# Kernel optimization log

Measured on AMD Instinct MI355X. Metric: run time of the kernel, lower is better.

Reference implementation:

```python
import jax, jax.numpy as jnp
import numpy as np

N = 50000          # total nodes
G = 16             # graphs in batch
NPG = N // G       # nodes per graph (3125)
E_RAND = 600000    # random intra-graph edges
EPG = E_RAND // G  # edges per graph
IN, HID, OUT = 128, 256, 256
LN_EPS = 1e-5


def setup_inputs() -> dict:
    key = jax.random.key(0)
    ks = jax.random.split(key, 20)
    features = jax.random.normal(ks[0], (N, IN), jnp.float32)
    # random edges constrained inside each graph block, then self loops (add_self_loop)
    off = (jnp.arange(E_RAND, dtype=jnp.int32) // EPG) * NPG
    src = jax.random.randint(ks[1], (E_RAND,), 0, NPG, dtype=jnp.int32) + off
    dst = jax.random.randint(ks[2], (E_RAND,), 0, NPG, dtype=jnp.int32) + off
    self_ids = jnp.arange(N, dtype=jnp.int32)
    edge_src = jnp.concatenate([src, self_ids])
    edge_dst = jnp.concatenate([dst, self_ids])
    graph_ids = (jnp.arange(N, dtype=jnp.int32) // NPG)

    def lin(k, i, o):
        return jax.random.normal(k, (i, o), jnp.float32) * 0.02

    dims = [(IN, HID), (HID, HID), (HID, OUT)]
    inp = {
        "features": features,
        "edge_src": edge_src,
        "edge_dst": edge_dst,
        "graph_ids": graph_ids,
    }
    for l, (di, do) in enumerate(dims):
        inp[f"Wself{l}"] = lin(ks[3 + 4 * l], di, do)
        inp[f"Wneigh{l}"] = lin(ks[4 + 4 * l], di, do)
        inp[f"b{l}"] = jnp.zeros((do,), jnp.float32)
        inp[f"g{l}"] = jnp.ones((do,), jnp.float32)
        inp[f"be{l}"] = jnp.zeros((do,), jnp.float32)
    return inp


def _layer_norm(x, g, b):
    m = jnp.mean(x, axis=-1, keepdims=True)
    v = jnp.mean((x - m) ** 2, axis=-1, keepdims=True)
    return (x - m) * jax.lax.rsqrt(v + LN_EPS) * g + b


def reference(features, edge_src, edge_dst, graph_ids,
              Wself0, Wneigh0, b0, g0, be0,
              Wself1, Wneigh1, b1, g1, be1,
              Wself2, Wneigh2, b2, g2, be2):
    n = features.shape[0]
    # in-degree (self loops guarantee >= 1)
    deg = jax.ops.segment_sum(jnp.ones_like(edge_dst, dtype=features.dtype), edge_dst, num_segments=n)
    deg_inv = (1.0 / deg)[:, None]

    def sage(h, Ws, Wn, b, g, be):
        # mean-aggregate neighbor (src) features at dst: gather + segment_sum
        agg = jax.ops.segment_sum(h[edge_src], edge_dst, num_segments=n) * deg_inv
        out = h @ Ws + agg @ Wn + b          # SAGEConv(mean): fc_self + fc_neigh
        return jax.nn.elu(_layer_norm(out, g, be))

    h = sage(features, Wself0, Wneigh0, b0, g0, be0)
    h = sage(h, Wself1, Wneigh1, b1, g1, be1)
    h = sage(h, Wself2, Wneigh2, b2, g2, be2)

    # per-graph mean readout (torch.mean over each graph's nodes)
    cnt = jax.ops.segment_sum(jnp.ones((n,), h.dtype), graph_ids, num_segments=G)
    hg = jax.ops.segment_sum(h, graph_ids, num_segments=G) / cnt[:, None]
    return h, hg
```

## Files before the change

### kernel.cpp

```cpp
#include <hip/hip_runtime.h>
#include <hip/hip_bf16.h>

constexpr int DOUT = 256;

typedef __bf16 bf16x8 __attribute__((ext_vector_type(8)));
typedef float f32x4 __attribute__((ext_vector_type(4)));

__device__ inline float bf2f(ushort u) {
  return __uint_as_float((unsigned)u << 16);
}
__device__ inline ushort f2bf(float f) {
  unsigned b = __float_as_uint(f);
  return (ushort)((b + 0x7FFF + ((b >> 16) & 1)) >> 16);
}
__device__ inline float bflo(int v) {
  return __uint_as_float((unsigned)v << 16);
}
__device__ inline float bfhi(int v) {
  return __uint_as_float((unsigned)v & 0xffff0000u);
}
__device__ inline int packbf(float a, float b) {
  return (int)((unsigned)f2bf(a) | ((unsigned)f2bf(b) << 16));
}

__device__ inline int xcd_swizzle(int bid, int nwg) {
  int q = nwg >> 3, r = nwg & 7;
  int xcd = bid & 7, idx = bid >> 3;
  return (xcd < r ? xcd * (q + 1) : r * (q + 1) + (xcd - r) * q) + idx;
}

__global__ __launch_bounds__(256) void k_cnt(const int* __restrict__ edst,
                                             int* __restrict__ deg, int E, int Eb,
                                             const int* __restrict__ gid,
                                             int* __restrict__ gcnt, int n, int G) {
  __shared__ int h[16];
  int b = blockIdx.x;
  if (b < Eb) {
    int t = b * 256 + threadIdx.x;
    if (t < E) atomicAdd(&deg[edst[t]], 1);
  } else {
    b -= Eb;
    int t = threadIdx.x;
    if (t < G) h[t] = 0;
    __syncthreads();
    int i = b * 256 + t;
    if (i < n) atomicAdd(&h[gid[i]], 1);
    __syncthreads();
    if (t < G && h[t]) atomicAdd(&gcnt[t], h[t]);
  }
}

__global__ __launch_bounds__(256) void k_scan1(const int* __restrict__ deg,
                                               int* __restrict__ part, int n) {
  int i = blockIdx.x * 256 + threadIdx.x;
  int v = (i < n) ? deg[i] : 0;
#pragma unroll
  for (int o = 32; o > 0; o >>= 1) v += __shfl_xor(v, o);
  __shared__ int s[4];
  int wave = threadIdx.x >> 6, lane = threadIdx.x & 63;
  if (lane == 0) s[wave] = v;
  __syncthreads();
  if (threadIdx.x == 0) part[blockIdx.x] = s[0] + s[1] + s[2] + s[3];
}

__global__ __launch_bounds__(256) void k_scan2(int* __restrict__ part, int nb) {
  __shared__ int s[256];
  int t = threadIdx.x;
  int v = (t < nb) ? part[t] : 0;
  s[t] = v;
  __syncthreads();
  for (int o = 1; o < 256; o <<= 1) {
    int u = (t >= o) ? s[t - o] : 0;
    __syncthreads();
    s[t] += u;
    __syncthreads();
  }
  int excl = (t == 0) ? 0 : s[t - 1];
  if (t < nb) part[t] = excl;
}

__global__ __launch_bounds__(256) void k_scan3(const int* __restrict__ deg,
                                               const int* __restrict__ part,
                                               int* __restrict__ rp,
                                               int* __restrict__ cur,
                                               float* __restrict__ dinv, int n) {
  __shared__ int s[256];
  int t = threadIdx.x;
  int i = blockIdx.x * 256 + t;
  int v = (i < n) ? deg[i] : 0;
  s[t] = v;
  __syncthreads();
  for (int o = 1; o < 256; o <<= 1) {
    int u = (t >= o) ? s[t - o] : 0;
    __syncthreads();
    s[t] += u;
    __syncthreads();
  }
  int incl = s[t];
  int excl = incl - v;
  int base = part[blockIdx.x];
  if (i < n) {
    rp[i] = base + excl;
    cur[i] = base + excl;
    dinv[i] = 1.0f / (float)v;
  }
  if (i == n - 1) rp[n] = base + incl;
}

__global__ __launch_bounds__(256) void k_fill(const int* __restrict__ src,
                                              const int* __restrict__ dst,
                                              int* __restrict__ cur,
                                              int* __restrict__ col, int E) {
  int e = blockIdx.x * 256 + threadIdx.x;
  if (e < E) {
    int p = atomicAdd(&cur[dst[e]], 1);
    col[p] = src[e];
  }
}

__global__ __launch_bounds__(256) void k_prep(
    const float* __restrict__ feat, ushort* __restrict__ feat_bf,
    long long feat4, int castb,
    const float* __restrict__ Ws0, const float* __restrict__ Wn0,
    ushort* __restrict__ Wt0, int DIN0,
    const float* __restrict__ Ws1, const float* __restrict__ Wn1,
    ushort* __restrict__ Wt1,
    const float* __restrict__ Ws2, const float* __restrict__ Wn2,
    ushort* __restrict__ Wt2) {
  int b = blockIdx.x;
  if (b < castb) {
    long long t = (long long)b * 256 + threadIdx.x;
    if (t < feat4) {
      float4 v = *(const float4*)(feat + t * 4);
      ushort4 o;
      o.x = f2bf(v.x); o.y = f2bf(v.y); o.z = f2bf(v.z); o.w = f2bf(v.w);
      *(ushort4*)(feat_bf + t * 4) = o;
    }
    return;
  }
  b -= castb;
  const float *Ws, *Wn;
  ushort* Wt;
  int DIN;
  if (b < 2 * DIN0) {
    Ws = Ws0; Wn = Wn0; Wt = Wt0; DIN = DIN0;
  } else if (b < 2 * DIN0 + 512) {
    b -= 2 * DIN0; Ws = Ws1; Wn = Wn1; Wt = Wt1; DIN = 256;
  } else {
    b -= 2 * DIN0 + 512; Ws = Ws2; Wn = Wn2; Wt = Wt2; DIN = 256;
  }
  int t = b * 256 + threadIdx.x;
  int K = 2 * DIN;
  int nn = t & 255;
  int k = t >> 8;
  if (k < K) {
    const float* W = (k < DIN) ? (Ws + (size_t)k * 256)
                               : (Wn + (size_t)(k - DIN) * 256);
    Wt[(size_t)nn * K + k] = f2bf(W[nn]);
  }
}

template <int DIN>
__global__ __launch_bounds__(256) void k_gather(const ushort* __restrict__ h,
                                                const int* __restrict__ rp,
                                                const int* __restrict__ col,
                                                const float* __restrict__ dinv,
                                                ushort* __restrict__ agg, int n) {
  int wg = xcd_swizzle(blockIdx.x, gridDim.x);
  int wave = threadIdx.x >> 6, lane = threadIdx.x & 63;
  int node = wg * 4 + wave;
  if (node >= n) return;
  int beg = rp[node], end = rp[node + 1];
  float s = dinv[node];
  int quad = lane >> 4, sub = lane & 15;
  if constexpr (DIN == 256) {
    const ushort* base = h + sub * 16;
    float a[16] = {};
    int j = beg + quad;
    for (; j + 4 < end; j += 8) {
      const ushort* p0 = base + (size_t)col[j] * DIN;
      const ushort* p1 = base + (size_t)col[j + 4] * DIN;
      int4 u0 = *(const int4*)p0;
      int4 u1 = *(const int4*)(p0 + 8);
      int4 v0 = *(const int4*)p1;
      int4 v1 = *(const int4*)(p1 + 8);
      a[0] += bflo(u0.x) + bflo(v0.x);  a[1] += bfhi(u0.x) + bfhi(v0.x);
      a[2] += bflo(u0.y) + bflo(v0.y);  a[3] += bfhi(u0.y) + bfhi(v0.y);
      a[4] += bflo(u0.z) + bflo(v0.z);  a[5] += bfhi(u0.z) + bfhi(v0.z);
      a[6] += bflo(u0.w) + bflo(v0.w);  a[7] += bfhi(u0.w) + bfhi(v0.w);
      a[8] += bflo(u1.x) + bflo(v1.x);  a[9] += bfhi(u1.x) + bfhi(v1.x);
      a[10] += bflo(u1.y) + bflo(v1.y); a[11] += bfhi(u1.y) + bfhi(v1.y);
      a[12] += bflo(u1.z) + bflo(v1.z); a[13] += bfhi(u1.z) + bfhi(v1.z);
      a[14] += bflo(u1.w) + bflo(v1.w); a[15] += bfhi(u1.w) + bfhi(v1.w);
    }
    for (; j < end; j += 4) {
      const ushort* p0 = base + (size_t)col[j] * DIN;
      int4 u0 = *(const int4*)p0;
      int4 u1 = *(const int4*)(p0 + 8);
      a[0] += bflo(u0.x);  a[1] += bfhi(u0.x);
      a[2] += bflo(u0.y);  a[3] += bfhi(u0.y);
      a[4] += bflo(u0.z);  a[5] += bfhi(u0.z);
      a[6] += bflo(u0.w);  a[7] += bfhi(u0.w);
      a[8] += bflo(u1.x);  a[9] += bfhi(u1.x);
      a[10] += bflo(u1.y); a[11] += bfhi(u1.y);
      a[12] += bflo(u1.z); a[13] += bfhi(u1.z);
      a[14] += bflo(u1.w); a[15] += bfhi(u1.w);
    }
#pragma unroll
    for (int d = 0; d < 16; ++d) {
      a[d] += __shfl_xor(a[d], 16);
      a[d] += __shfl_xor(a[d], 32);
    }
    if (quad == 0) {
      ushort* op = agg + (size_t)node * DIN + sub * 16;
      int4 o0, o1;
      o0.x = packbf(a[0] * s, a[1] * s);
      o0.y = packbf(a[2] * s, a[3] * s);
      o0.z = packbf(a[4] * s, a[5] * s);
      o0.w = packbf(a[6] * s, a[7] * s);
      o1.x = packbf(a[8] * s, a[9] * s);
      o1.y = packbf(a[10] * s, a[11] * s);
      o1.z = packbf(a[12] * s, a[13] * s);
      o1.w = packbf(a[14] * s, a[15] * s);
      *(int4*)op = o0;
      *(int4*)(op + 8) = o1;
    }
  } else {
    const ushort* base = h + sub * 8;
    float a[8] = {};
    int j = beg + quad;
    for (; j + 4 < end; j += 8) {
      int4 v0 = *(const int4*)(base + (size_t)col[j] * DIN);
      int4 v1 = *(const int4*)(base + (size_t)col[j + 4] * DIN);
      a[0] += bflo(v0.x) + bflo(v1.x);
      a[1] += bfhi(v0.x) + bfhi(v1.x);
      a[2] += bflo(v0.y) + bflo(v1.y);
      a[3] += bfhi(v0.y) + bfhi(v1.y);
      a[4] += bflo(v0.z) + bflo(v1.z);
      a[5] += bfhi(v0.z) + bfhi(v1.z);
      a[6] += bflo(v0.w) + bflo(v1.w);
      a[7] += bfhi(v0.w) + bfhi(v1.w);
    }
    for (; j < end; j += 4) {
      int4 v = *(const int4*)(base + (size_t)col[j] * DIN);
      a[0] += bflo(v.x); a[1] += bfhi(v.x);
      a[2] += bflo(v.y); a[3] += bfhi(v.y);
      a[4] += bflo(v.z); a[5] += bfhi(v.z);
      a[6] += bflo(v.w); a[7] += bfhi(v.w);
    }
#pragma unroll
    for (int d = 0; d < 8; ++d) {
      a[d] += __shfl_xor(a[d], 16);
      a[d] += __shfl_xor(a[d], 32);
    }
    if (quad == 0) {
      int4 o;
      o.x = packbf(a[0] * s, a[1] * s);
      o.y = packbf(a[2] * s, a[3] * s);
      o.z = packbf(a[4] * s, a[5] * s);
      o.w = packbf(a[6] * s, a[7] * s);
      *(int4*)(agg + (size_t)node * DIN + sub * 8) = o;
    }
  }
}

template <int DIN, bool BF16OUT, bool READOUT>
__global__ __launch_bounds__(512) void k_gemm_ln(
    const ushort* __restrict__ A0, const ushort* __restrict__ A1,
    const ushort* __restrict__ Wt, const float* __restrict__ bias,
    const float* __restrict__ g, const float* __restrict__ be,
    ushort* __restrict__ outB, float* __restrict__ outF, int n,
    float* __restrict__ out_hg, int npg, int G) {
  constexpr int K = 2 * DIN;
  __shared__ ushort As[128 * 32];
  __shared__ ushort Bs[256 * 32];
  __shared__ float redS[4][128];
  __shared__ float redQ[4][128];
  __shared__ float hgp[2][256];
  const int tid = threadIdx.x;
  const int lane = tid & 63, wid = tid >> 6;
  const int wr = wid >> 2, wc = wid & 3;
  const int m0 = blockIdx.x * 128;
  const int fr = lane & 15, kg = lane >> 4;
  const int s_row = tid >> 2, s_c = tid & 3;

  f32x4 acc[4][4] = {};

  for (int k0 = 0; k0 < K; k0 += 32) {
    const ushort* Asrc = (k0 < DIN) ? A0 : A1;
    const int ak = (k0 < DIN) ? k0 : (k0 - DIN);
    {
      int grow = m0 + s_row;
      int4 v = make_int4(0, 0, 0, 0);
      if (grow < n) v = *(const int4*)(Asrc + (size_t)grow * DIN + ak + s_c * 8);
      *(int4*)&As[s_row * 32 + ((s_c ^ ((s_row >> 1) & 3)) * 8)] = v;
      int4 w0 = *(const int4*)(Wt + (size_t)s_row * K + k0 + s_c * 8);
      *(int4*)&Bs[s_row * 32 + ((s_c ^ ((s_row >> 1) & 3)) * 8)] = w0;
      int r2 = s_row + 128;
      int4 w1 = *(const int4*)(Wt + (size_t)r2 * K + k0 + s_c * 8);
      *(int4*)&Bs[r2 * 32 + ((s_c ^ ((r2 >> 1) & 3)) * 8)] = w1;
    }
    __syncthreads();
    bf16x8 af[4], bb[4];
#pragma unroll
    for (int mi = 0; mi < 4; ++mi) {
      int row = wr * 64 + mi * 16 + fr;
      af[mi] = *(const bf16x8*)&As[row * 32 + ((kg ^ ((row >> 1) & 3)) * 8)];
    }
#pragma unroll
    for (int ni = 0; ni < 4; ++ni) {
      int row = wc * 64 + ni * 16 + fr;
      bb[ni] = *(const bf16x8*)&Bs[row * 32 + ((kg ^ ((row >> 1) & 3)) * 8)];
    }
#pragma unroll
    for (int mi = 0; mi < 4; ++mi)
#pragma unroll
      for (int ni = 0; ni < 4; ++ni)
        acc[mi][ni] = __builtin_amdgcn_mfma_f32_16x16x32_bf16(af[mi], bb[ni],
                                                              acc[mi][ni], 0, 0, 0);
    __syncthreads();
  }

  float bv[4], gv[4], ev[4];
#pragma unroll
  for (int ni = 0; ni < 4; ++ni) {
    int c = wc * 64 + ni * 16 + fr;
    bv[ni] = bias[c];
    gv[ni] = g[c];
    ev[ni] = be[c];
  }
#pragma unroll
  for (int mi = 0; mi < 4; ++mi)
#pragma unroll
    for (int ni = 0; ni < 4; ++ni)
#pragma unroll
      for (int j = 0; j < 4; ++j) acc[mi][ni][j] += bv[ni];

#pragma unroll
  for (int mi = 0; mi < 4; ++mi) {
#pragma unroll
    for (int j = 0; j < 4; ++j) {
      float s = 0.f, q = 0.f;
#pragma unroll
      for (int ni = 0; ni < 4; ++ni) {
        float a = acc[mi][ni][j];
        s += a;
        q += a * a;
      }
#pragma unroll
      for (int o = 1; o < 16; o <<= 1) {
        s += __shfl_xor(s, o);
        q += __shfl_xor(q, o);
      }
      if (fr == 0) {
        int lr = wr * 64 + mi * 16 + kg * 4 + j;
        redS[wc][lr] = s;
        redQ[wc][lr] = q;
      }
    }
  }
  if constexpr (READOUT) ((float*)hgp)[tid < 512 ? tid : 0] = 0.f;
  __syncthreads();

  const int g0 = m0 / npg;
  const int b1 = (g0 + 1) * npg;
  float s0[4] = {}, s1[4] = {};
#pragma unroll
  for (int mi = 0; mi < 4; ++mi) {
#pragma unroll
    for (int j = 0; j < 4; ++j) {
      int lr = wr * 64 + mi * 16 + kg * 4 + j;
      int r = m0 + lr;
      if (r >= n) continue;
      float tot = redS[0][lr] + redS[1][lr] + redS[2][lr] + redS[3][lr];
      float tq = redQ[0][lr] + redQ[1][lr] + redQ[2][lr] + redQ[3][lr];
      float mean = tot * (1.0f / 256.0f);
      float var = tq * (1.0f / 256.0f) - mean * mean;
      float rstd = rsqrtf(var + 1e-5f);
#pragma unroll
      for (int ni = 0; ni < 4; ++ni) {
        int c = wc * 64 + ni * 16 + fr;
        float val = (acc[mi][ni][j] - mean) * rstd * gv[ni] + ev[ni];
        val = val > 0.f ? val : expm1f(val);
        if constexpr (BF16OUT)
          outB[(size_t)r * DOUT + c] = f2bf(val);
        else
          outF[(size_t)r * DOUT + c] = val;
        if constexpr (READOUT) {
          if (r < b1) s0[ni] += val; else s1[ni] += val;
        }
      }
    }
  }
  if constexpr (READOUT) {
#pragma unroll
    for (int ni = 0; ni < 4; ++ni) {
      int c = wc * 64 + ni * 16 + fr;
      if (s0[ni] != 0.f) atomicAdd(&hgp[0][c], s0[ni]);
      if (s1[ni] != 0.f) atomicAdd(&hgp[1][c], s1[ni]);
    }
    __syncthreads();
    if (tid < 256) {
      float v = hgp[0][tid];
      if (v != 0.f) atomicAdd(&out_hg[(size_t)g0 * DOUT + tid], v);
    } else {
      float v = hgp[1][tid - 256];
      if (v != 0.f && g0 + 1 < G)
        atomicAdd(&out_hg[(size_t)(g0 + 1) * DOUT + (tid - 256)], v);
    }
  }
}

__global__ __launch_bounds__(256) void k_hg_scale(float* __restrict__ hg,
                                                  const int* __restrict__ cnt,
                                                  int total) {
  int t = blockIdx.x * blockDim.x + threadIdx.x;
  if (t < total) hg[t] *= 1.0f / (float)cnt[t >> 8];
}

extern "C" void kernel_launch(void* const* d_in, const int* in_sizes, int n_in,
                              void* d_out, int out_size, void* d_ws, size_t ws_size,
                              hipStream_t stream) {
  const float* feat = (const float*)d_in[0];
  const int* esrc = (const int*)d_in[1];
  const int* edst = (const int*)d_in[2];
  const int* gid = (const int*)d_in[3];
  const float* Ws0 = (const float*)d_in[4];
  const float* Wn0 = (const float*)d_in[5];
  const float* b0 = (const float*)d_in[6];
  const float* g0 = (const float*)d_in[7];
  const float* be0 = (const float*)d_in[8];
  const float* Ws1 = (const float*)d_in[9];
  const float* Wn1 = (const float*)d_in[10];
  const float* b1 = (const float*)d_in[11];
  const float* g1 = (const float*)d_in[12];
  const float* be1 = (const float*)d_in[13];
  const float* Ws2 = (const float*)d_in[14];
  const float* Wn2 = (const float*)d_in[15];
  const float* b2 = (const float*)d_in[16];
  const float* g2 = (const float*)d_in[17];
  const float* be2 = (const float*)d_in[18];

  const int E = in_sizes[1];
  const int n = in_sizes[3];
  const int DIN0 = in_sizes[0] / n;
  const int Gn = (out_size - n * DOUT) / DOUT;
  const int npg = n / Gn;
  const int nb = (n + 255) / 256;
  const int Eb = (E + 255) / 256;

  char* ws = (char*)d_ws;
  size_t off = 0;
  auto alloc = [&](size_t bytes) -> void* {
    void* p = ws + off;
    off += (bytes + 255) & ~(size_t)255;
    return p;
  };
  int* deg_cnt = (int*)alloc((size_t)n * 4);
  int* gcnt = (int*)alloc((size_t)Gn * 4);
  size_t cnt_span = off;
  float* dinv = (float*)alloc((size_t)n * 4);
  int* row_ptr = (int*)alloc((size_t)(n + 1) * 4);
  int* cursor = (int*)alloc((size_t)n * 4);
  int* part = (int*)alloc((size_t)nb * 4);
  int* col = (int*)alloc((size_t)E * 4);
  ushort* feat_bf = (ushort*)alloc((size_t)n * DIN0 * 2);
  ushort* h_bf = (ushort*)alloc((size_t)n * DOUT * 2);
  ushort* agg_bf = (ushort*)alloc((size_t)n * DOUT * 2);
  ushort* Wt0 = (ushort*)alloc((size_t)256 * 2 * DIN0 * 2);
  ushort* Wt1 = (ushort*)alloc((size_t)256 * 2 * DOUT * 2);
  ushort* Wt2 = (ushort*)alloc((size_t)256 * 2 * DOUT * 2);

  float* out_h = (float*)d_out;
  float* out_hg = out_h + (size_t)n * DOUT;

  hipMemsetAsync(deg_cnt, 0, cnt_span, stream);
  hipMemsetAsync(out_hg, 0, (size_t)Gn * DOUT * 4, stream);

  k_cnt<<<Eb + nb, 256, 0, stream>>>(edst, deg_cnt, E, Eb, gid, gcnt, n, Gn);

  k_scan1<<<nb, 256, 0, stream>>>(deg_cnt, part, n);
  k_scan2<<<1, 256, 0, stream>>>(part, nb);
  k_scan3<<<nb, 256, 0, stream>>>(deg_cnt, part, row_ptr, cursor, dinv, n);
  k_fill<<<Eb, 256, 0, stream>>>(esrc, edst, cursor, col, E);

  const long long feat4 = (long long)n * DIN0 / 4;
  const int castb = (int)((feat4 + 255) / 256);
  k_prep<<<castb + 2 * DIN0 + 1024, 256, 0, stream>>>(
      feat, feat_bf, feat4, castb, Ws0, Wn0, Wt0, DIN0, Ws1, Wn1, Wt1, Ws2,
      Wn2, Wt2);

  int gemm_grid = (n + 127) / 128;
  int row_grid = (n + 3) / 4;

  k_gather<128><<<row_grid, 256, 0, stream>>>(feat_bf, row_ptr, col, dinv,
                                              agg_bf, n);
  k_gemm_ln<128, true, false><<<gemm_grid, 512, 0, stream>>>(
      feat_bf, agg_bf, Wt0, b0, g0, be0, h_bf, nullptr, n, nullptr, npg, Gn);

  k_gather<256><<<row_grid, 256, 0, stream>>>(h_bf, row_ptr, col, dinv,
                                              agg_bf, n);
  k_gemm_ln<256, true, false><<<gemm_grid, 512, 0, stream>>>(
      h_bf, agg_bf, Wt1, b1, g1, be1, h_bf, nullptr, n, nullptr, npg, Gn);

  k_gather<256><<<row_grid, 256, 0, stream>>>(h_bf, row_ptr, col, dinv,
                                              agg_bf, n);
  k_gemm_ln<256, false, true><<<gemm_grid, 512, 0, stream>>>(
      h_bf, agg_bf, Wt2, b2, g2, be2, nullptr, out_h, n, out_hg, npg, Gn);

  k_hg_scale<<<(Gn * DOUT + 255) / 256, 256, 0, stream>>>(out_hg, gcnt,
                                                          Gn * DOUT);
}
```

Measured before the change: 278.8 us.

## Double-buffer GEMM-LN tiles via direct global-to-LDS loads with 64-row blocks

Rewrites the fused GEMM+LayerNorm kernel to use 64-row tiles with 256 threads, each wave owning a 64-column slice. Tiles are loaded straight into double-buffered LDS with global_load_lds so the next K-tile's fetch overlaps the current MFMA step, dropping one barrier per iteration. The smaller tile doubles the grid for more occupancy, but each block now reloads the full weight tile for fewer rows, so weight traffic per output row doubles. The A row index is clamped to n-1 instead of zero-filled.

```diff
diff --git a/kernel.cpp b/kernel.cpp
--- a/kernel.cpp
+++ b/kernel.cpp
@@ -21,6 +21,12 @@
 }
 __device__ inline int packbf(float a, float b) {
   return (int)((unsigned)f2bf(a) | ((unsigned)f2bf(b) << 16));
+}
+
+__device__ inline void gload_lds16(const ushort* g, ushort* l) {
+  __builtin_amdgcn_global_load_lds(
+      (const __attribute__((address_space(1))) unsigned int*)g,
+      (__attribute__((address_space(3))) unsigned int*)l, 16, 0, 0);
 }
 
 __device__ inline int xcd_swizzle(int bid, int nwg) {
@@ -265,52 +271,57 @@
 }
 
 template <int DIN, bool BF16OUT, bool READOUT>
-__global__ __launch_bounds__(512) void k_gemm_ln(
+__global__ __launch_bounds__(256) void k_gemm_ln(
     const ushort* __restrict__ A0, const ushort* __restrict__ A1,
     const ushort* __restrict__ Wt, const float* __restrict__ bias,
     const float* __restrict__ g, const float* __restrict__ be,
     ushort* __restrict__ outB, float* __restrict__ outF, int n,
     float* __restrict__ out_hg, int npg, int G) {
   constexpr int K = 2 * DIN;
-  __shared__ ushort As[128 * 32];
-  __shared__ ushort Bs[256 * 32];
-  __shared__ float redS[4][128];
-  __shared__ float redQ[4][128];
+  constexpr int NT = K / 32;
+  __shared__ ushort As[2][64 * 32];
+  __shared__ ushort Bs[2][256 * 32];
+  __shared__ float redS[4][64];
+  __shared__ float redQ[4][64];
   __shared__ float hgp[2][256];
   const int tid = threadIdx.x;
-  const int lane = tid & 63, wid = tid >> 6;
-  const int wr = wid >> 2, wc = wid & 3;
-  const int m0 = blockIdx.x * 128;
+  const int lane = tid & 63, w = tid >> 6;
+  const int m0 = blockIdx.x * 64;
   const int fr = lane & 15, kg = lane >> 4;
-  const int s_row = tid >> 2, s_c = tid & 3;
+  const int lr4 = lane >> 2;
+  const int lc = (lane & 3) ^ ((lane >> 3) & 3);
+  const int arow = min(m0 + w * 16 + lr4, n - 1);
 
   f32x4 acc[4][4] = {};
 
-  for (int k0 = 0; k0 < K; k0 += 32) {
+  auto stage = [&](int buf, int t) {
+    int k0 = t * 32;
     const ushort* Asrc = (k0 < DIN) ? A0 : A1;
-    const int ak = (k0 < DIN) ? k0 : (k0 - DIN);
-    {
-      int grow = m0 + s_row;
-      int4 v = make_int4(0, 0, 0, 0);
-      if (grow < n) v = *(const int4*)(Asrc + (size_t)grow * DIN + ak + s_c * 8);
-      *(int4*)&As[s_row * 32 + ((s_c ^ ((s_row >> 1) & 3)) * 8)] = v;
-      int4 w0 = *(const int4*)(Wt + (size_t)s_row * K + k0 + s_c * 8);
-      *(int4*)&Bs[s_row * 32 + ((s_c ^ ((s_row >> 1) & 3)) * 8)] = w0;
-      int r2 = s_row + 128;
-      int4 w1 = *(const int4*)(Wt + (size_t)r2 * K + k0 + s_c * 8);
-      *(int4*)&Bs[r2 * 32 + ((s_c ^ ((r2 >> 1) & 3)) * 8)] = w1;
-    }
-    __syncthreads();
+    int ak = (k0 < DIN) ? k0 : (k0 - DIN);
+    gload_lds16(Asrc + (size_t)arow * DIN + ak + lc * 8, &As[buf][w * 512]);
+#pragma unroll
+    for (int q = 0; q < 4; ++q) {
+      int row = w * 64 + q * 16 + lr4;
+      gload_lds16(Wt + (size_t)row * K + k0 + lc * 8,
+                  &Bs[buf][(w * 64 + q * 16) * 32]);
+    }
+  };
+
+  stage(0, 0);
+  __syncthreads();
+  int cur = 0;
+  for (int t = 0; t < NT; ++t) {
+    if (t + 1 < NT) stage(cur ^ 1, t + 1);
     bf16x8 af[4], bb[4];
 #pragma unroll
     for (int mi = 0; mi < 4; ++mi) {
-      int row = wr * 64 + mi * 16 + fr;
-      af[mi] = *(const bf16x8*)&As[row * 32 + ((kg ^ ((row >> 1) & 3)) * 8)];
+      int row = mi * 16 + fr;
+      af[mi] = *(const bf16x8*)&As[cur][row * 32 + ((kg ^ ((row >> 1) & 3)) * 8)];
     }
 #pragma unroll
     for (int ni = 0; ni < 4; ++ni) {
-      int row = wc * 64 + ni * 16 + fr;
-      bb[ni] = *(const bf16x8*)&Bs[row * 32 + ((kg ^ ((row >> 1) & 3)) * 8)];
+      int row = w * 64 + ni * 16 + fr;
+      bb[ni] = *(const bf16x8*)&Bs[cur][row * 32 + ((kg ^ ((row >> 1) & 3)) * 8)];
     }
 #pragma unroll
     for (int mi = 0; mi < 4; ++mi)
@@ -319,12 +330,13 @@
         acc[mi][ni] = __builtin_amdgcn_mfma_f32_16x16x32_bf16(af[mi], bb[ni],
                                                               acc[mi][ni], 0, 0, 0);
     __syncthreads();
+    cur ^= 1;
   }
 
   float bv[4], gv[4], ev[4];
 #pragma unroll
   for (int ni = 0; ni < 4; ++ni) {
-    int c = wc * 64 + ni * 16 + fr;
+    int c = w * 64 + ni * 16 + fr;
     bv[ni] = bias[c];
     gv[ni] = g[c];
     ev[ni] = be[c];
@@ -353,13 +365,16 @@
         q += __shfl_xor(q, o);
       }
       if (fr == 0) {
-        int lr = wr * 64 + mi * 16 + kg * 4 + j;
-        redS[wc][lr] = s;
-        redQ[wc][lr] = q;
+        int lr = mi * 16 + kg * 4 + j;
+        redS[w][lr] = s;
+        redQ[w][lr] = q;
       }
     }
   }
-  if constexpr (READOUT) ((float*)hgp)[tid < 512 ? tid : 0] = 0.f;
+  if constexpr (READOUT) {
+    ((float*)hgp)[tid] = 0.f;
+    ((float*)hgp)[tid + 256] = 0.f;
+  }
   __syncthreads();
 
   const int g0 = m0 / npg;
@@ -369,7 +384,7 @@
   for (int mi = 0; mi < 4; ++mi) {
 #pragma unroll
     for (int j = 0; j < 4; ++j) {
-      int lr = wr * 64 + mi * 16 + kg * 4 + j;
+      int lr = mi * 16 + kg * 4 + j;
       int r = m0 + lr;
       if (r >= n) continue;
       float tot = redS[0][lr] + redS[1][lr] + redS[2][lr] + redS[3][lr];
@@ -379,7 +394,7 @@
       float rstd = rsqrtf(var + 1e-5f);
 #pragma unroll
       for (int ni = 0; ni < 4; ++ni) {
-        int c = wc * 64 + ni * 16 + fr;
+        int c = w * 64 + ni * 16 + fr;
         float val = (acc[mi][ni][j] - mean) * rstd * gv[ni] + ev[ni];
         val = val > 0.f ? val : expm1f(val);
         if constexpr (BF16OUT)
@@ -395,19 +410,16 @@
   if constexpr (READOUT) {
 #pragma unroll
     for (int ni = 0; ni < 4; ++ni) {
-      int c = wc * 64 + ni * 16 + fr;
+      int c = w * 64 + ni * 16 + fr;
       if (s0[ni] != 0.f) atomicAdd(&hgp[0][c], s0[ni]);
       if (s1[ni] != 0.f) atomicAdd(&hgp[1][c], s1[ni]);
     }
     __syncthreads();
-    if (tid < 256) {
-      float v = hgp[0][tid];
-      if (v != 0.f) atomicAdd(&out_hg[(size_t)g0 * DOUT + tid], v);
-    } else {
-      float v = hgp[1][tid - 256];
-      if (v != 0.f && g0 + 1 < G)
-        atomicAdd(&out_hg[(size_t)(g0 + 1) * DOUT + (tid - 256)], v);
-    }
+    float v0 = hgp[0][tid];
+    if (v0 != 0.f) atomicAdd(&out_hg[(size_t)g0 * DOUT + tid], v0);
+    float v1 = hgp[1][tid];
+    if (v1 != 0.f && g0 + 1 < G)
+      atomicAdd(&out_hg[(size_t)(g0 + 1) * DOUT + tid], v1);
   }
 }
 
@@ -490,22 +502,22 @@
       feat, feat_bf, feat4, castb, Ws0, Wn0, Wt0, DIN0, Ws1, Wn1, Wt1, Ws2,
       Wn2, Wt2);
 
-  int gemm_grid = (n + 127) / 128;
+  int gemm_grid = (n + 63) / 64;
   int row_grid = (n + 3) / 4;
 
   k_gather<128><<<row_grid, 256, 0, stream>>>(feat_bf, row_ptr, col, dinv,
                                               agg_bf, n);
-  k_gemm_ln<128, true, false><<<gemm_grid, 512, 0, stream>>>(
+  k_gemm_ln<128, true, false><<<gemm_grid, 256, 0, stream>>>(
       feat_bf, agg_bf, Wt0, b0, g0, be0, h_bf, nullptr, n, nullptr, npg, Gn);
 
   k_gather<256><<<row_grid, 256, 0, stream>>>(h_bf, row_ptr, col, dinv,
                                               agg_bf, n);
-  k_gemm_ln<256, true, false><<<gemm_grid, 512, 0, stream>>>(
+  k_gemm_ln<256, true, false><<<gemm_grid, 256, 0, stream>>>(
       h_bf, agg_bf, Wt1, b1, g1, be1, h_bf, nullptr, n, nullptr, npg, Gn);
 
   k_gather<256><<<row_grid, 256, 0, stream>>>(h_bf, row_ptr, col, dinv,
                                               agg_bf, n);
-  k_gemm_ln<256, false, true><<<gemm_grid, 512, 0, stream>>>(
+  k_gemm_ln<256, false, true><<<gemm_grid, 256, 0, stream>>>(
       h_bf, agg_bf, Wt2, b2, g2, be2, nullptr, out_h, n, out_hg, npg, Gn);
 
   k_hg_scale<<<(Gn * DOUT + 255) / 256, 256, 0, stream>>>(out_hg, gcnt,
```

Result: slower. 310.0 us (+11.2%).
